# Optimization experiments

Hardware: AMD Instinct MI355X
Metric: run time of the kernel (lower is better)

Reference implementation:

```python
import jax, jax.numpy as jnp
import numpy as np

B, S, D, H = 8, 1024, 1024, 16
DH = D // H
LN_EPS = 1e-5
SLOPE = 0.01  # nn.LeakyReLU default negative_slope


def _ln(x, g, b):
    m = x.mean(-1, keepdims=True)
    v = ((x - m) ** 2).mean(-1, keepdims=True)
    return (x - m) / jnp.sqrt(v + LN_EPS) * g + b


def _leaky(x):
    return jnp.where(x >= 0, x, SLOPE * x)


def setup_inputs() -> dict:
    key = jax.random.key(0)
    ks = jax.random.split(key, 6)
    q = jax.random.normal(ks[0], (B, S, D), dtype=jnp.float32)
    masks = jnp.ones((B, S), dtype=jnp.int32)  # all-valid mask (masked_fill is a no-op)
    w1 = jax.random.normal(ks[1], (D, D), dtype=jnp.float32) * 0.02
    b1 = jnp.zeros((D,), jnp.float32)
    w2 = jax.random.normal(ks[2], (D, D), dtype=jnp.float32) * 0.02
    b2 = jnp.zeros((D,), jnp.float32)
    ones = jnp.ones((D,), jnp.float32)
    zeros = jnp.zeros((D,), jnp.float32)
    return dict(q=q, masks=masks,
                w1=w1, b1=b1, ln1_g=ones, ln1_b=zeros,
                w2=w2, b2=b2, ln2_g=ones, ln2_b=zeros,
                anf_g=ones, anf_b=zeros,
                an1_g=ones, an1_b=zeros,
                an2_g=ones, an2_b=zeros)


def reference(q, masks, w1, b1, ln1_g, ln1_b, w2, b2, ln2_g, ln2_b,
              anf_g, anf_b, an1_g, an1_b, an2_g, an2_b):
    # --- multi-head cosine-similarity attention (k = v = q, no projections) ---
    qh = q.reshape(B, S, H, DH).transpose(0, 2, 1, 3)  # (B,H,S,DH) == separate_heads
    qn = qh / jnp.clip(jnp.linalg.norm(qh, axis=-1, keepdims=True), 1e-8)
    # cosine similarity scores, softmax over keys
    w = jax.nn.softmax(jnp.einsum('bhqd,bhkd->bhqk', qn, qn), axis=-1)
    # masked_fill AFTER softmax (faithful to source: mask per (batch, query))
    w = jnp.where(masks[:, None, :, None] == 0, jnp.float32(-1e9), w)
    heads = jnp.einsum('bhqk,bhkd->bhqd', w, qh)
    attn = heads.transpose(0, 2, 1, 3).reshape(B, S, D)  # concat_heads
    # --- add_norm1 (dropout=0.5 but eval mode => identity) ---
    y1 = _ln(q + attn, an1_g, an1_b)
    # --- PositionWiseFFN: Linear->LN->LeakyReLU x2, then internal AddNorm ---
    h = _leaky(_ln(y1 @ w1 + b1, ln1_g, ln1_b))
    y = _leaky(_ln(h @ w2 + b2, ln2_g, ln2_b))
    y2 = _ln(y1 + y, anf_g, anf_b)
    # --- add_norm2 ---
    return _ln(y1 + y2, an2_g, an2_b)
```

## Files before the change

kernel.cpp:

```cpp
#include <hip/hip_runtime.h>
#include <hip/hip_bf16.h>

#define BB 8
#define SS 1024
#define DD 1024
#define HH 16

typedef __attribute__((ext_vector_type(8))) short short8;
typedef __attribute__((ext_vector_type(8))) __bf16 bf16x8;
typedef __attribute__((ext_vector_type(4))) float f32x4;

__device__ inline float bf2f(unsigned short h){
  unsigned u = ((unsigned)h) << 16;
  return __builtin_bit_cast(float, u);
}
__device__ inline unsigned short f2bf(float f){
  unsigned u = __builtin_bit_cast(unsigned, f);
  u += 0x7fffu + ((u >> 16) & 1u);
  return (unsigned short)(u >> 16);
}
__device__ inline f32x4 mfma16(short8 a, short8 b, f32x4 c){
  return __builtin_amdgcn_mfma_f32_16x16x32_bf16(
      __builtin_bit_cast(bf16x8, a), __builtin_bit_cast(bf16x8, b), c, 0, 0, 0);
}
__device__ inline void gld_lds16(const unsigned short* g, unsigned short* l){
  __builtin_amdgcn_global_load_lds((const __attribute__((address_space(1))) void*)g,
      (__attribute__((address_space(3))) void*)l, 16, 0, 0);
}

__global__ __launch_bounds__(256) void prep_w(const float* __restrict__ w1,
                                              const float* __restrict__ w2,
                                              unsigned short* __restrict__ w1T,
                                              unsigned short* __restrict__ w2T){
  __shared__ float tile[64][65];
  const float* src = blockIdx.z ? w2 : w1;
  unsigned short* dst = blockIdx.z ? w2T : w1T;
  int k0 = blockIdx.x * 64, n0 = blockIdx.y * 64;
  int tx = threadIdx.x & 63, ty = threadIdx.x >> 6;
#pragma unroll
  for (int r = 0; r < 16; ++r)
    tile[ty + 4*r][tx] = src[(k0 + ty + 4*r) * DD + n0 + tx];
  __syncthreads();
#pragma unroll
  for (int r = 0; r < 16; ++r)
    dst[(n0 + ty + 4*r) * DD + k0 + tx] = f2bf(tile[tx][ty + 4*r]);
}

__global__ __launch_bounds__(256) void prep_q(const float* __restrict__ q,
                                              unsigned short* __restrict__ kf,
                                              unsigned short* __restrict__ vf,
                                              unsigned short* __restrict__ qb){
  __shared__ float tile[64][65];
  __shared__ float rinv[64];
  int bh = blockIdx.x >> 4, st = blockIdx.x & 15;
  int b = bh >> 4, h = bh & 15;
  int t = threadIdx.x;
  int tx = t & 63, ty = t >> 6;
  int srow = b * SS + st * 64;
#pragma unroll
  for (int r = 0; r < 16; ++r)
    tile[ty + 4*r][tx] = q[(size_t)(srow + ty + 4*r) * DD + h * 64 + tx];
  __syncthreads();
  {
    int s = t >> 2, p = t & 3;
    float ssum = 0.f;
#pragma unroll
    for (int i = 0; i < 16; ++i){ float v = tile[s][p*16 + i]; ssum += v * v; }
    ssum += __shfl_xor(ssum, 1);
    ssum += __shfl_xor(ssum, 2);
    if (p == 0) rinv[s] = 1.0f / fmaxf(sqrtf(ssum), 1e-8f);
  }
  __syncthreads();
#pragma unroll
  for (int r = 0; r < 16; ++r)
    qb[(size_t)(srow + ty + 4*r) * DD + h * 64 + tx] = f2bf(tile[ty + 4*r][tx]);
#pragma unroll
  for (int v = 0; v < 2; ++v){
    int idx = t * 2 + v;
    int c_l = idx >> 6, lane = idx & 63;
    int g2 = c_l >> 2, c = (c_l >> 1) & 1, hf = c_l & 1;
    int lrq = lane & 15, lgq = lane >> 4;
    int s = g2 * 32 + (lrq >> 2) * 8 + c * 4 + (lrq & 3);
    int d0 = hf * 32 + lgq * 8;
    float rv = rinv[s] * 1.20112240878645f;
    short8 o;
#pragma unroll
    for (int e = 0; e < 8; ++e) o[e] = (short)f2bf(tile[s][d0 + e] * rv);
    *(short8*)(kf + ((size_t)(bh * 128 + st * 8 + c_l) * 64 + lane) * 8) = o;
  }
#pragma unroll
  for (int v = 0; v < 2; ++v){
    int idx = t * 2 + v;
    int kt2 = idx >> 8, db = (idx >> 6) & 3, lane = idx & 63;
    int d = db * 16 + (lane & 15);
    int k0 = kt2 * 32 + (lane >> 4) * 8;
    short8 o;
#pragma unroll
    for (int e = 0; e < 8; ++e) o[e] = (short)f2bf(tile[k0 + e][d]);
    *(short8*)(vf + ((size_t)((bh * 32 + st * 2 + kt2) * 4 + db) * 512 + lane * 8)) = o;
  }
}

#define NPH 16
__global__ __launch_bounds__(512, 4) void attn_kern(const unsigned short* __restrict__ kf,
                                                    const unsigned short* __restrict__ vf,
                                                    const int* __restrict__ masks,
                                                    unsigned short* __restrict__ attnb){
  __shared__ unsigned short Kb[3][8][512];
  __shared__ unsigned short Vb[3][8][512];
  __shared__ int anym;
  const int bh = blockIdx.x, b = bh >> 4, h = bh & 15;
  const int by = blockIdx.y;
  const int t = threadIdx.x, w = t >> 6, l = t & 63;
  const int lr = l & 15, lg = l >> 4;
  if (t == 0) anym = 0;
  __syncthreads();
  if (t < 256 && masks[b * SS + by * 256 + t] == 0) anym = 1;

  short8 aQ[2][2];
#pragma unroll
  for (int c = 0; c < 2; ++c)
#pragma unroll
    for (int hf = 0; hf < 2; ++hf)
      aQ[c][hf] = *(const short8*)(kf +
          ((size_t)(bh * 128 + (by * 8 + w) * 4 + c * 2 + hf) * 64 + l) * 8);

  const short ONEB = (short)0x3F80;
  const short8 ones = {ONEB, ONEB, ONEB, ONEB, ONEB, ONEB, ONEB, ONEB};

#define STAGE(ph, bf) do {                                                            \
    if (w < 4){                                                                       \
      gld_lds16(kf + ((size_t)(bh * 128 + (2*(ph)) * 4 + w) * 64 + l) * 8,            \
                &Kb[bf][w][0]);                                                       \
      gld_lds16(kf + ((size_t)(bh * 128 + (2*(ph)+1) * 4 + w) * 64 + l) * 8,          \
                &Kb[bf][4 + w][0]);                                                   \
    } else {                                                                          \
      gld_lds16(vf + ((size_t)((bh * 32 + 2*(ph)) * 4 + (w - 4)) * 512 + l * 8),      \
                &Vb[bf][w - 4][0]);                                                   \
      gld_lds16(vf + ((size_t)((bh * 32 + 2*(ph)+1) * 4 + (w - 4)) * 512 + l * 8),    \
                &Vb[bf][4 + (w - 4)][0]);                                             \
    }                                                                                 \
  } while (0)

  STAGE(0, 0);
  STAGE(1, 1);
  asm volatile("s_waitcnt vmcnt(2) lgkmcnt(0)" ::: "memory");
  __builtin_amdgcn_s_barrier();

  f32x4 o[2][4] = {};
  f32x4 rsacc[2] = {};

  for (int ph = 0; ph < NPH; ++ph){
    const int cur = ph % 3;
    if (ph + 2 < NPH) STAGE(ph + 2, (ph + 2) % 3);
#pragma unroll
    for (int gi = 0; gi < 2; ++gi){
      short8 bK[2][2];
#pragma unroll
      for (int c = 0; c < 2; ++c)
#pragma unroll
        for (int hf = 0; hf < 2; ++hf)
          bK[c][hf] = *(const short8*)&Kb[cur][gi * 4 + c * 2 + hf][l * 8];
      f32x4 sc[2][2];
#pragma unroll
      for (int qc = 0; qc < 2; ++qc)
#pragma unroll
        for (int c = 0; c < 2; ++c){
          f32x4 z = {0.f, 0.f, 0.f, 0.f};
          z = mfma16(bK[c][0], aQ[qc][0], z);
          z = mfma16(bK[c][1], aQ[qc][1], z);
          sc[qc][c] = z;
        }
      bf16x8 pav[2];
#pragma unroll
      for (int qc = 0; qc < 2; ++qc)
#pragma unroll
        for (int c = 0; c < 2; ++c)
#pragma unroll
          for (int j = 0; j < 4; ++j){
            float x = sc[qc][c][j], pv;
            asm("v_exp_f32 %0, %1" : "=v"(pv) : "v"(x));
            pav[qc][c * 4 + j] = (__bf16)pv;
          }
      short8 pa0 = __builtin_bit_cast(short8, pav[0]);
      short8 pa1 = __builtin_bit_cast(short8, pav[1]);
      rsacc[0] = mfma16(pa0, ones, rsacc[0]);
      rsacc[1] = mfma16(pa1, ones, rsacc[1]);
#pragma unroll
      for (int db = 0; db < 4; ++db){
        short8 bV = *(const short8*)&Vb[cur][gi * 4 + db][l * 8];
        o[0][db] = mfma16(pa0, bV, o[0][db]);
        o[1][db] = mfma16(pa1, bV, o[1][db]);
      }
    }
    if (ph + 1 < NPH){
      asm volatile("s_waitcnt lgkmcnt(0)" ::: "memory");
      if (ph + 2 < NPH) asm volatile("s_waitcnt vmcnt(2)" ::: "memory");
      else              asm volatile("s_waitcnt vmcnt(0)" ::: "memory");
      __builtin_amdgcn_s_barrier();
    }
  }

#pragma unroll
  for (int qc = 0; qc < 2; ++qc){
    float invj[4];
#pragma unroll
    for (int j = 0; j < 4; ++j) invj[j] = 1.0f / rsacc[qc][j];
#pragma unroll
    for (int db = 0; db < 4; ++db)
#pragma unroll
      for (int j = 0; j < 4; ++j){
        int qrow = by * 256 + w * 32 + lg * 8 + qc * 4 + j;
        float val = o[qc][db][j] * invj[j];
        if (anym && masks[b * SS + qrow] == 0){
          float vs = 0.f;
          for (int kt = 0; kt < 32; ++kt)
            for (int lgp = 0; lgp < 4; ++lgp){
              const unsigned short* vp = vf +
                  ((size_t)((bh * 32 + kt) * 4 + db) * 512 + (lgp * 16 + lr) * 8);
              for (int e = 0; e < 8; ++e) vs += bf2f(vp[e]);
            }
          val = -1e9f * vs;
        }
        attnb[(size_t)(b * SS + qrow) * DD + h * 64 + db * 16 + lr] = f2bf(val);
      }
  }
#undef STAGE
}

__device__ inline float2 block_reduce2(float a, float bq){
  __shared__ float sm[8];
#pragma unroll
  for (int off = 1; off < 64; off <<= 1){
    a += __shfl_xor(a, off);
    bq += __shfl_xor(bq, off);
  }
  int w = threadIdx.x >> 6;
  if ((threadIdx.x & 63) == 0){ sm[2*w] = a; sm[2*w + 1] = bq; }
  __syncthreads();
  float2 r;
  r.x = sm[0] + sm[2] + sm[4] + sm[6];
  r.y = sm[1] + sm[3] + sm[5] + sm[7];
  __syncthreads();
  return r;
}

__global__ __launch_bounds__(256) void addnorm1(const unsigned short* __restrict__ qb,
                                                const unsigned short* __restrict__ attnb,
                                                const float* __restrict__ g,
                                                const float* __restrict__ bt,
                                                unsigned short* __restrict__ y1b){
  int row = blockIdx.x, t = threadIdx.x;
  ushort4 qv = *(const ushort4*)(qb + (size_t)row * DD + t * 4);
  ushort4 av = *(const ushort4*)(attnb + (size_t)row * DD + t * 4);
  float x[4] = { bf2f(qv.x) + bf2f(av.x), bf2f(qv.y) + bf2f(av.y),
                 bf2f(qv.z) + bf2f(av.z), bf2f(qv.w) + bf2f(av.w) };
  float s = 0.f, ssq = 0.f;
#pragma unroll
  for (int i = 0; i < 4; ++i){ s += x[i]; ssq += x[i] * x[i]; }
  float2 r = block_reduce2(s, ssq);
  float m = r.x * (1.0f / DD);
  float rs = rsqrtf(r.y * (1.0f / DD) - m * m + 1e-5f);
  float4 gv = *(const float4*)(g + t * 4);
  float4 bv = *(const float4*)(bt + t * 4);
  float y[4] = { (x[0]-m)*rs*gv.x + bv.x, (x[1]-m)*rs*gv.y + bv.y,
                 (x[2]-m)*rs*gv.z + bv.z, (x[3]-m)*rs*gv.w + bv.w };
  ushort4 ob = { f2bf(y[0]), f2bf(y[1]), f2bf(y[2]), f2bf(y[3]) };
  *(ushort4*)(y1b + (size_t)row * DD + t * 4) = ob;
}

__global__ __launch_bounds__(256, 2) void gemm_bias(const unsigned short* __restrict__ X,
                                                    const unsigned short* __restrict__ WT,
                                                    const float* __restrict__ bias,
                                                    unsigned short* __restrict__ out){
  __shared__ unsigned short As[3][128 * 32];
  __shared__ unsigned short Bs[3][128 * 32];
  int t = threadIdx.x, l = t & 63, w = t >> 6;
  int wm = w >> 1, wn = w & 1;
  int lr = l & 15, lg = l >> 4;
  int bm = blockIdx.x * 128, bn = blockIdx.y * 128;
  f32x4 acc[4][4] = {};
  int r = t >> 2, cb = (t & 3) * 8;

#define GSTAGE(kt, bf) do {                                                        \
    gld_lds16(X  + (size_t)(bm +      r) * 1024 + (kt) * 32 + cb,                  \
              &As[bf][w * 512]);                                                   \
    gld_lds16(X  + (size_t)(bm + 64 + r) * 1024 + (kt) * 32 + cb,                  \
              &As[bf][2048 + w * 512]);                                            \
    gld_lds16(WT + (size_t)(bn +      r) * 1024 + (kt) * 32 + cb,                  \
              &Bs[bf][w * 512]);                                                   \
    gld_lds16(WT + (size_t)(bn + 64 + r) * 1024 + (kt) * 32 + cb,                  \
              &Bs[bf][2048 + w * 512]);                                            \
  } while (0)

  GSTAGE(0, 0);
  GSTAGE(1, 1);
  asm volatile("s_waitcnt vmcnt(4)" ::: "memory");
  __builtin_amdgcn_s_barrier();

  for (int kt = 0; kt < 32; ++kt){
    const int cur = kt % 3;
    if (kt + 2 < 32) GSTAGE(kt + 2, (kt + 2) % 3);
    short8 aA[4], bB[4];
#pragma unroll
    for (int i = 0; i < 4; ++i)
      aA[i] = *(const short8*)&As[cur][(wm * 64 + i * 16 + lr) * 32 + lg * 8];
#pragma unroll
    for (int i = 0; i < 4; ++i)
      bB[i] = *(const short8*)&Bs[cur][(wn * 64 + i * 16 + lr) * 32 + lg * 8];
#pragma unroll
    for (int mi = 0; mi < 4; ++mi)
#pragma unroll
      for (int ni = 0; ni < 4; ++ni)
        acc[mi][ni] = mfma16(aA[mi], bB[ni], acc[mi][ni]);
    if (kt + 1 < 32){
      asm volatile("s_waitcnt lgkmcnt(0)" ::: "memory");
      if (kt + 2 < 32) asm volatile("s_waitcnt vmcnt(4)" ::: "memory");
      else             asm volatile("s_waitcnt vmcnt(0)" ::: "memory");
      __builtin_amdgcn_s_barrier();
    }
  }
#undef GSTAGE
#pragma unroll
  for (int ni = 0; ni < 4; ++ni){
    int col = bn + wn * 64 + ni * 16 + lr;
    float bv = bias[col];
#pragma unroll
    for (int mi = 0; mi < 4; ++mi){
      int row0 = bm + wm * 64 + mi * 16 + lg * 4;
#pragma unroll
      for (int j = 0; j < 4; ++j)
        out[(size_t)(row0 + j) * 1024 + col] = f2bf(acc[mi][ni][j] + bv);
    }
  }
}

__global__ __launch_bounds__(256) void ln_leaky(const unsigned short* __restrict__ in,
                                                const float* __restrict__ g,
                                                const float* __restrict__ bt,
                                                unsigned short* __restrict__ out){
  int row = blockIdx.x, t = threadIdx.x;
  ushort4 iv = *(const ushort4*)(in + (size_t)row * DD + t * 4);
  float x[4] = { bf2f(iv.x), bf2f(iv.y), bf2f(iv.z), bf2f(iv.w) };
  float s = 0.f, ssq = 0.f;
#pragma unroll
  for (int i = 0; i < 4; ++i){ s += x[i]; ssq += x[i] * x[i]; }
  float2 r = block_reduce2(s, ssq);
  float m = r.x * (1.0f / DD);
  float rs = rsqrtf(r.y * (1.0f / DD) - m * m + 1e-5f);
  float4 gv = *(const float4*)(g + t * 4);
  float4 bv = *(const float4*)(bt + t * 4);
  ushort4 ov;
  {
    float v0 = (x[0]-m)*rs*gv.x + bv.x; v0 = v0 >= 0.f ? v0 : 0.01f*v0; ov.x = f2bf(v0);
    float v1 = (x[1]-m)*rs*gv.y + bv.y; v1 = v1 >= 0.f ? v1 : 0.01f*v1; ov.y = f2bf(v1);
    float v2 = (x[2]-m)*rs*gv.z + bv.z; v2 = v2 >= 0.f ? v2 : 0.01f*v2; ov.z = f2bf(v2);
    float v3 = (x[3]-m)*rs*gv.w + bv.w; v3 = v3 >= 0.f ? v3 : 0.01f*v3; ov.w = f2bf(v3);
  }
  *(ushort4*)(out + (size_t)row * DD + t * 4) = ov;
}

__global__ __launch_bounds__(256) void final_kern(const unsigned short* __restrict__ g2,
                                                  const unsigned short* __restrict__ y1,
                                                  const float* __restrict__ ln2g, const float* __restrict__ ln2b,
                                                  const float* __restrict__ anfg, const float* __restrict__ anfb,
                                                  const float* __restrict__ an2g, const float* __restrict__ an2b,
                                                  float* __restrict__ out){
  int row = blockIdx.x, t = threadIdx.x;
  ushort4 iv = *(const ushort4*)(g2 + (size_t)row * DD + t * 4);
  ushort4 y1v = *(const ushort4*)(y1 + (size_t)row * DD + t * 4);
  float x[4] = { bf2f(iv.x), bf2f(iv.y), bf2f(iv.z), bf2f(iv.w) };
  float yy1[4] = { bf2f(y1v.x), bf2f(y1v.y), bf2f(y1v.z), bf2f(y1v.w) };
  float s = 0.f, ssq = 0.f;
#pragma unroll
  for (int i = 0; i < 4; ++i){ s += x[i]; ssq += x[i]*x[i]; }
  float2 r = block_reduce2(s, ssq);
  float m = r.x * (1.0f / DD);
  float rs = rsqrtf(r.y * (1.0f / DD) - m*m + 1e-5f);
  float4 gv = *(const float4*)(ln2g + t * 4);
  float4 bv = *(const float4*)(ln2b + t * 4);
  float y[4] = { (x[0]-m)*rs*gv.x + bv.x, (x[1]-m)*rs*gv.y + bv.y,
                 (x[2]-m)*rs*gv.z + bv.z, (x[3]-m)*rs*gv.w + bv.w };
#pragma unroll
  for (int i = 0; i < 4; ++i) y[i] = y[i] >= 0.f ? y[i] : 0.01f*y[i];

  float tv[4]; s = 0.f; ssq = 0.f;
#pragma unroll
  for (int i = 0; i < 4; ++i){ tv[i] = yy1[i] + y[i]; s += tv[i]; ssq += tv[i]*tv[i]; }
  r = block_reduce2(s, ssq);
  m = r.x * (1.0f / DD);
  rs = rsqrtf(r.y * (1.0f / DD) - m*m + 1e-5f);
  gv = *(const float4*)(anfg + t * 4);
  bv = *(const float4*)(anfb + t * 4);
  float y2[4] = { (tv[0]-m)*rs*gv.x + bv.x, (tv[1]-m)*rs*gv.y + bv.y,
                  (tv[2]-m)*rs*gv.z + bv.z, (tv[3]-m)*rs*gv.w + bv.w };

  float u[4]; s = 0.f; ssq = 0.f;
#pragma unroll
  for (int i = 0; i < 4; ++i){ u[i] = yy1[i] + y2[i]; s += u[i]; ssq += u[i]*u[i]; }
  r = block_reduce2(s, ssq);
  m = r.x * (1.0f / DD);
  rs = rsqrtf(r.y * (1.0f / DD) - m*m + 1e-5f);
  gv = *(const float4*)(an2g + t * 4);
  bv = *(const float4*)(an2b + t * 4);
  float4 ov = { (u[0]-m)*rs*gv.x + bv.x, (u[1]-m)*rs*gv.y + bv.y,
                (u[2]-m)*rs*gv.z + bv.z, (u[3]-m)*rs*gv.w + bv.w };
  *(float4*)(out + (size_t)row * DD + t * 4) = ov;
}

extern "C" void kernel_launch(void* const* d_in, const int* in_sizes, int n_in,
                              void* d_out, int out_size, void* d_ws, size_t ws_size,
                              hipStream_t stream){
  const float* q    = (const float*)d_in[0];
  const int* masks  = (const int*)d_in[1];
  const float* w1   = (const float*)d_in[2];
  const float* b1   = (const float*)d_in[3];
  const float* ln1g = (const float*)d_in[4];
  const float* ln1b = (const float*)d_in[5];
  const float* w2   = (const float*)d_in[6];
  const float* b2   = (const float*)d_in[7];
  const float* ln2g = (const float*)d_in[8];
  const float* ln2b = (const float*)d_in[9];
  const float* anfg = (const float*)d_in[10];
  const float* anfb = (const float*)d_in[11];
  const float* an1g = (const float*)d_in[12];
  const float* an1b = (const float*)d_in[13];
  const float* an2g = (const float*)d_in[14];
  const float* an2b = (const float*)d_in[15];

  char* ws = (char*)d_ws;
  unsigned short* w1T  = (unsigned short*)(ws + 0);
  unsigned short* w2T  = (unsigned short*)(ws + 2097152);
  unsigned short* kf   = (unsigned short*)(ws + 4194304);
  unsigned short* vf   = (unsigned short*)(ws + 20971520);
  unsigned short* attn = (unsigned short*)(ws + 37748736);
  unsigned short* y1b  = (unsigned short*)(ws + 54525952);
  unsigned short* qb   = (unsigned short*)(ws + 71303168);
  unsigned short* g1   = kf;
  unsigned short* hbuf = vf;
  unsigned short* g2   = attn;
  float* outp = (float*)d_out;

  prep_w<<<dim3(16, 16, 2), 256, 0, stream>>>(w1, w2, w1T, w2T);
  prep_q<<<dim3(2048), 256, 0, stream>>>(q, kf, vf, qb);
  attn_kern<<<dim3(128, 4), 512, 0, stream>>>(kf, vf, masks, attn);
  addnorm1<<<dim3(8192), 256, 0, stream>>>(qb, attn, an1g, an1b, y1b);
  gemm_bias<<<dim3(64, 8), 256, 0, stream>>>(y1b, w1T, b1, g1);
  ln_leaky<<<dim3(8192), 256, 0, stream>>>(g1, ln1g, ln1b, hbuf);
  gemm_bias<<<dim3(64, 8), 256, 0, stream>>>(hbuf, w2T, b2, g2);
  final_kern<<<dim3(8192), 256, 0, stream>>>(g2, y1b, ln2g, ln2b, anfg, anfb, an2g, an2b, outp);
}
```

Before: 155.1 us.

## Stage GEMM output through LDS, vectorize row-norm kernels to two rows per block

The GEMM epilogue now writes bias-added bf16 results into the shared-memory buffer, then copies them out as coalesced 16-byte row stores instead of scattered 2-byte stores. The MFMA loop is wrapped in s_setprio to favour the math waves. The three layer-norm kernels now process two rows per 256-thread block with 8-element vector loads and a half-block reduction, halving their grid size. The added barriers and LDS round trip cost a little time in the GEMM epilogue.

```diff
diff --git a/kernel.cpp b/kernel.cpp
--- a/kernel.cpp
+++ b/kernel.cpp
@@ -228,7 +228,7 @@
 #undef STAGE
 }
 
-__device__ inline float2 block_reduce2(float a, float bq){
+__device__ inline float2 br2(float a, float bq){
   __shared__ float sm[8];
 #pragma unroll
   for (int off = 1; off < 64; off <<= 1){
@@ -236,11 +236,12 @@
     bq += __shfl_xor(bq, off);
   }
   int w = threadIdx.x >> 6;
-  if ((threadIdx.x & 63) == 0){ sm[2*w] = a; sm[2*w + 1] = bq; }
-  __syncthreads();
+  if ((threadIdx.x & 63) == 0){ sm[w * 2] = a; sm[w * 2 + 1] = bq; }
+  __syncthreads();
+  int base = (threadIdx.x >> 7) * 4;
   float2 r;
-  r.x = sm[0] + sm[2] + sm[4] + sm[6];
-  r.y = sm[1] + sm[3] + sm[5] + sm[7];
+  r.x = sm[base] + sm[base + 2];
+  r.y = sm[base + 1] + sm[base + 3];
   __syncthreads();
   return r;
 }
@@ -250,31 +251,34 @@
                                                 const float* __restrict__ g,
                                                 const float* __restrict__ bt,
                                                 unsigned short* __restrict__ y1b){
-  int row = blockIdx.x, t = threadIdx.x;
-  ushort4 qv = *(const ushort4*)(qb + (size_t)row * DD + t * 4);
-  ushort4 av = *(const ushort4*)(attnb + (size_t)row * DD + t * 4);
-  float x[4] = { bf2f(qv.x) + bf2f(av.x), bf2f(qv.y) + bf2f(av.y),
-                 bf2f(qv.z) + bf2f(av.z), bf2f(qv.w) + bf2f(av.w) };
-  float s = 0.f, ssq = 0.f;
-#pragma unroll
-  for (int i = 0; i < 4; ++i){ s += x[i]; ssq += x[i] * x[i]; }
-  float2 r = block_reduce2(s, ssq);
+  int rg = threadIdx.x >> 7, tt = threadIdx.x & 127;
+  int row = blockIdx.x * 2 + rg;
+  short8 qv = *(const short8*)(qb + (size_t)row * DD + tt * 8);
+  short8 av = *(const short8*)(attnb + (size_t)row * DD + tt * 8);
+  float x[8]; float s = 0.f, ssq = 0.f;
+#pragma unroll
+  for (int i = 0; i < 8; ++i){
+    x[i] = bf2f((unsigned short)qv[i]) + bf2f((unsigned short)av[i]);
+    s += x[i]; ssq += x[i] * x[i];
+  }
+  float2 r = br2(s, ssq);
   float m = r.x * (1.0f / DD);
   float rs = rsqrtf(r.y * (1.0f / DD) - m * m + 1e-5f);
-  float4 gv = *(const float4*)(g + t * 4);
-  float4 bv = *(const float4*)(bt + t * 4);
-  float y[4] = { (x[0]-m)*rs*gv.x + bv.x, (x[1]-m)*rs*gv.y + bv.y,
-                 (x[2]-m)*rs*gv.z + bv.z, (x[3]-m)*rs*gv.w + bv.w };
-  ushort4 ob = { f2bf(y[0]), f2bf(y[1]), f2bf(y[2]), f2bf(y[3]) };
-  *(ushort4*)(y1b + (size_t)row * DD + t * 4) = ob;
+  float4 g0 = *(const float4*)(g + tt * 8), g1 = *(const float4*)(g + tt * 8 + 4);
+  float4 b0 = *(const float4*)(bt + tt * 8), b1 = *(const float4*)(bt + tt * 8 + 4);
+  float gg[8] = {g0.x,g0.y,g0.z,g0.w,g1.x,g1.y,g1.z,g1.w};
+  float bb[8] = {b0.x,b0.y,b0.z,b0.w,b1.x,b1.y,b1.z,b1.w};
+  short8 ob;
+#pragma unroll
+  for (int i = 0; i < 8; ++i) ob[i] = (short)f2bf((x[i]-m)*rs*gg[i] + bb[i]);
+  *(short8*)(y1b + (size_t)row * DD + tt * 8) = ob;
 }
 
 __global__ __launch_bounds__(256, 2) void gemm_bias(const unsigned short* __restrict__ X,
                                                     const unsigned short* __restrict__ WT,
                                                     const float* __restrict__ bias,
                                                     unsigned short* __restrict__ out){
-  __shared__ unsigned short As[3][128 * 32];
-  __shared__ unsigned short Bs[3][128 * 32];
+  __shared__ unsigned short LDSB[24576];
   int t = threadIdx.x, l = t & 63, w = t >> 6;
   int wm = w >> 1, wn = w & 1;
   int lr = l & 15, lg = l >> 4;
@@ -282,15 +286,17 @@
   f32x4 acc[4][4] = {};
   int r = t >> 2, cb = (t & 3) * 8;
 
+#define ASP(bf) (LDSB + (bf) * 4096)
+#define BSP(bf) (LDSB + 12288 + (bf) * 4096)
 #define GSTAGE(kt, bf) do {                                                        \
     gld_lds16(X  + (size_t)(bm +      r) * 1024 + (kt) * 32 + cb,                  \
-              &As[bf][w * 512]);                                                   \
+              ASP(bf) + w * 512);                                                  \
     gld_lds16(X  + (size_t)(bm + 64 + r) * 1024 + (kt) * 32 + cb,                  \
-              &As[bf][2048 + w * 512]);                                            \
+              ASP(bf) + 2048 + w * 512);                                           \
     gld_lds16(WT + (size_t)(bn +      r) * 1024 + (kt) * 32 + cb,                  \
-              &Bs[bf][w * 512]);                                                   \
+              BSP(bf) + w * 512);                                                  \
     gld_lds16(WT + (size_t)(bn + 64 + r) * 1024 + (kt) * 32 + cb,                  \
-              &Bs[bf][2048 + w * 512]);                                            \
+              BSP(bf) + 2048 + w * 512);                                           \
   } while (0)
 
   GSTAGE(0, 0);
@@ -304,15 +310,17 @@
     short8 aA[4], bB[4];
 #pragma unroll
     for (int i = 0; i < 4; ++i)
-      aA[i] = *(const short8*)&As[cur][(wm * 64 + i * 16 + lr) * 32 + lg * 8];
+      aA[i] = *(const short8*)(ASP(cur) + (wm * 64 + i * 16 + lr) * 32 + lg * 8);
 #pragma unroll
     for (int i = 0; i < 4; ++i)
-      bB[i] = *(const short8*)&Bs[cur][(wn * 64 + i * 16 + lr) * 32 + lg * 8];
+      bB[i] = *(const short8*)(BSP(cur) + (wn * 64 + i * 16 + lr) * 32 + lg * 8);
+    __builtin_amdgcn_s_setprio(1);
 #pragma unroll
     for (int mi = 0; mi < 4; ++mi)
 #pragma unroll
       for (int ni = 0; ni < 4; ++ni)
         acc[mi][ni] = mfma16(aA[mi], bB[ni], acc[mi][ni]);
+    __builtin_amdgcn_s_setprio(0);
     if (kt + 1 < 32){
       asm volatile("s_waitcnt lgkmcnt(0)" ::: "memory");
       if (kt + 2 < 32) asm volatile("s_waitcnt vmcnt(4)" ::: "memory");
@@ -321,43 +329,63 @@
     }
   }
 #undef GSTAGE
+
+  asm volatile("s_waitcnt lgkmcnt(0)" ::: "memory");
+  __builtin_amdgcn_s_barrier();
 #pragma unroll
   for (int ni = 0; ni < 4; ++ni){
-    int col = bn + wn * 64 + ni * 16 + lr;
-    float bv = bias[col];
+    int col = wn * 64 + ni * 16 + lr;
+    float bv = bias[bn + col];
 #pragma unroll
     for (int mi = 0; mi < 4; ++mi){
-      int row0 = bm + wm * 64 + mi * 16 + lg * 4;
+      int row0 = wm * 64 + mi * 16 + lg * 4;
 #pragma unroll
       for (int j = 0; j < 4; ++j)
-        out[(size_t)(row0 + j) * 1024 + col] = f2bf(acc[mi][ni][j] + bv);
+        LDSB[(row0 + j) * 128 + col] = f2bf(acc[mi][ni][j] + bv);
     }
   }
+  asm volatile("s_waitcnt lgkmcnt(0)" ::: "memory");
+  __builtin_amdgcn_s_barrier();
+#pragma unroll
+  for (int i = 0; i < 8; ++i){
+    int idx = t + i * 256;
+    int row = idx >> 4;
+    int c8  = idx & 15;
+    short8 v = *(const short8*)&LDSB[row * 128 + c8 * 8];
+    *(short8*)(out + (size_t)(bm + row) * 1024 + bn + c8 * 8) = v;
+  }
+#undef ASP
+#undef BSP
 }
 
 __global__ __launch_bounds__(256) void ln_leaky(const unsigned short* __restrict__ in,
                                                 const float* __restrict__ g,
                                                 const float* __restrict__ bt,
                                                 unsigned short* __restrict__ out){
-  int row = blockIdx.x, t = threadIdx.x;
-  ushort4 iv = *(const ushort4*)(in + (size_t)row * DD + t * 4);
-  float x[4] = { bf2f(iv.x), bf2f(iv.y), bf2f(iv.z), bf2f(iv.w) };
-  float s = 0.f, ssq = 0.f;
-#pragma unroll
-  for (int i = 0; i < 4; ++i){ s += x[i]; ssq += x[i] * x[i]; }
-  float2 r = block_reduce2(s, ssq);
+  int rg = threadIdx.x >> 7, tt = threadIdx.x & 127;
+  int row = blockIdx.x * 2 + rg;
+  short8 iv = *(const short8*)(in + (size_t)row * DD + tt * 8);
+  float x[8]; float s = 0.f, ssq = 0.f;
+#pragma unroll
+  for (int i = 0; i < 8; ++i){
+    x[i] = bf2f((unsigned short)iv[i]);
+    s += x[i]; ssq += x[i] * x[i];
+  }
+  float2 r = br2(s, ssq);
   float m = r.x * (1.0f / DD);
   float rs = rsqrtf(r.y * (1.0f / DD) - m * m + 1e-5f);
-  float4 gv = *(const float4*)(g + t * 4);
-  float4 bv = *(const float4*)(bt + t * 4);
-  ushort4 ov;
-  {
-    float v0 = (x[0]-m)*rs*gv.x + bv.x; v0 = v0 >= 0.f ? v0 : 0.01f*v0; ov.x = f2bf(v0);
-    float v1 = (x[1]-m)*rs*gv.y + bv.y; v1 = v1 >= 0.f ? v1 : 0.01f*v1; ov.y = f2bf(v1);
-    float v2 = (x[2]-m)*rs*gv.z + bv.z; v2 = v2 >= 0.f ? v2 : 0.01f*v2; ov.z = f2bf(v2);
-    float v3 = (x[3]-m)*rs*gv.w + bv.w; v3 = v3 >= 0.f ? v3 : 0.01f*v3; ov.w = f2bf(v3);
-  }
-  *(ushort4*)(out + (size_t)row * DD + t * 4) = ov;
+  float4 g0 = *(const float4*)(g + tt * 8), g1 = *(const float4*)(g + tt * 8 + 4);
+  float4 b0 = *(const float4*)(bt + tt * 8), b1 = *(const float4*)(bt + tt * 8 + 4);
+  float gg[8] = {g0.x,g0.y,g0.z,g0.w,g1.x,g1.y,g1.z,g1.w};
+  float bb[8] = {b0.x,b0.y,b0.z,b0.w,b1.x,b1.y,b1.z,b1.w};
+  short8 ov;
+#pragma unroll
+  for (int i = 0; i < 8; ++i){
+    float v = (x[i]-m)*rs*gg[i] + bb[i];
+    v = v >= 0.f ? v : 0.01f * v;
+    ov[i] = (short)f2bf(v);
+  }
+  *(short8*)(out + (size_t)row * DD + tt * 8) = ov;
 }
 
 __global__ __launch_bounds__(256) void final_kern(const unsigned short* __restrict__ g2,
@@ -366,46 +394,62 @@
                                                   const float* __restrict__ anfg, const float* __restrict__ anfb,
                                                   const float* __restrict__ an2g, const float* __restrict__ an2b,
                                                   float* __restrict__ out){
-  int row = blockIdx.x, t = threadIdx.x;
-  ushort4 iv = *(const ushort4*)(g2 + (size_t)row * DD + t * 4);
-  ushort4 y1v = *(const ushort4*)(y1 + (size_t)row * DD + t * 4);
-  float x[4] = { bf2f(iv.x), bf2f(iv.y), bf2f(iv.z), bf2f(iv.w) };
-  float yy1[4] = { bf2f(y1v.x), bf2f(y1v.y), bf2f(y1v.z), bf2f(y1v.w) };
-  float s = 0.f, ssq = 0.f;
-#pragma unroll
-  for (int i = 0; i < 4; ++i){ s += x[i]; ssq += x[i]*x[i]; }
-  float2 r = block_reduce2(s, ssq);
+  int rg = threadIdx.x >> 7, tt = threadIdx.x & 127;
+  int row = blockIdx.x * 2 + rg;
+  short8 iv = *(const short8*)(g2 + (size_t)row * DD + tt * 8);
+  short8 yv = *(const short8*)(y1 + (size_t)row * DD + tt * 8);
+  float x[8], yy1[8]; float s = 0.f, ssq = 0.f;
+#pragma unroll
+  for (int i = 0; i < 8; ++i){
+    x[i] = bf2f((unsigned short)iv[i]);
+    yy1[i] = bf2f((unsigned short)yv[i]);
+    s += x[i]; ssq += x[i] * x[i];
+  }
+  float2 r = br2(s, ssq);
   float m = r.x * (1.0f / DD);
-  float rs = rsqrtf(r.y * (1.0f / DD) - m*m + 1e-5f);
-  float4 gv = *(const float4*)(ln2g + t * 4);
-  float4 bv = *(const float4*)(ln2b + t * 4);
-  float y[4] = { (x[0]-m)*rs*gv.x + bv.x, (x[1]-m)*rs*gv.y + bv.y,
-                 (x[2]-m)*rs*gv.z + bv.z, (x[3]-m)*rs*gv.w + bv.w };
-#pragma unroll
-  for (int i = 0; i < 4; ++i) y[i] = y[i] >= 0.f ? y[i] : 0.01f*y[i];
-
-  float tv[4]; s = 0.f; ssq = 0.f;
-#pragma unroll
-  for (int i = 0; i < 4; ++i){ tv[i] = yy1[i] + y[i]; s += tv[i]; ssq += tv[i]*tv[i]; }
-  r = block_reduce2(s, ssq);
+  float rs = rsqrtf(r.y * (1.0f / DD) - m * m + 1e-5f);
+  float4 p0, p1;
+  p0 = *(const float4*)(ln2g + tt * 8); p1 = *(const float4*)(ln2g + tt * 8 + 4);
+  float gg[8] = {p0.x,p0.y,p0.z,p0.w,p1.x,p1.y,p1.z,p1.w};
+  p0 = *(const float4*)(ln2b + tt * 8); p1 = *(const float4*)(ln2b + tt * 8 + 4);
+  float bb[8] = {p0.x,p0.y,p0.z,p0.w,p1.x,p1.y,p1.z,p1.w};
+  float y[8];
+#pragma unroll
+  for (int i = 0; i < 8; ++i){
+    float v = (x[i]-m)*rs*gg[i] + bb[i];
+    y[i] = v >= 0.f ? v : 0.01f * v;
+  }
+
+  float tv[8]; s = 0.f; ssq = 0.f;
+#pragma unroll
+  for (int i = 0; i < 8; ++i){ tv[i] = yy1[i] + y[i]; s += tv[i]; ssq += tv[i]*tv[i]; }
+  r = br2(s, ssq);
   m = r.x * (1.0f / DD);
   rs = rsqrtf(r.y * (1.0f / DD) - m*m + 1e-5f);
-  gv = *(const float4*)(anfg + t * 4);
-  bv = *(const float4*)(anfb + t * 4);
-  float y2[4] = { (tv[0]-m)*rs*gv.x + bv.x, (tv[1]-m)*rs*gv.y + bv.y,
-                  (tv[2]-m)*rs*gv.z + bv.z, (tv[3]-m)*rs*gv.w + bv.w };
-
-  float u[4]; s = 0.f; ssq = 0.f;
-#pragma unroll
-  for (int i = 0; i < 4; ++i){ u[i] = yy1[i] + y2[i]; s += u[i]; ssq += u[i]*u[i]; }
-  r = block_reduce2(s, ssq);
+  p0 = *(const float4*)(anfg + tt * 8); p1 = *(const float4*)(anfg + tt * 8 + 4);
+  float gg2[8] = {p0.x,p0.y,p0.z,p0.w,p1.x,p1.y,p1.z,p1.w};
+  p0 = *(const float4*)(anfb + tt * 8); p1 = *(const float4*)(anfb + tt * 8 + 4);
+  float bb2[8] = {p0.x,p0.y,p0.z,p0.w,p1.x,p1.y,p1.z,p1.w};
+  float y2[8];
+#pragma unroll
+  for (int i = 0; i < 8; ++i) y2[i] = (tv[i]-m)*rs*gg2[i] + bb2[i];
+
+  float u[8]; s = 0.f; ssq = 0.f;
+#pragma unroll
+  for (int i = 0; i < 8; ++i){ u[i] = yy1[i] + y2[i]; s += u[i]; ssq += u[i]*u[i]; }
+  r = br2(s, ssq);
   m = r.x * (1.0f / DD);
   rs = rsqrtf(r.y * (1.0f / DD) - m*m + 1e-5f);
-  gv = *(const float4*)(an2g + t * 4);
-  bv = *(const float4*)(an2b + t * 4);
-  float4 ov = { (u[0]-m)*rs*gv.x + bv.x, (u[1]-m)*rs*gv.y + bv.y,
-                (u[2]-m)*rs*gv.z + bv.z, (u[3]-m)*rs*gv.w + bv.w };
-  *(float4*)(out + (size_t)row * DD + t * 4) = ov;
+  p0 = *(const float4*)(an2g + tt * 8); p1 = *(const float4*)(an2g + tt * 8 + 4);
+  float gg3[8] = {p0.x,p0.y,p0.z,p0.w,p1.x,p1.y,p1.z,p1.w};
+  p0 = *(const float4*)(an2b + tt * 8); p1 = *(const float4*)(an2b + tt * 8 + 4);
+  float bb3[8] = {p0.x,p0.y,p0.z,p0.w,p1.x,p1.y,p1.z,p1.w};
+  float4 o0 = { (u[0]-m)*rs*gg3[0] + bb3[0], (u[1]-m)*rs*gg3[1] + bb3[1],
+                (u[2]-m)*rs*gg3[2] + bb3[2], (u[3]-m)*rs*gg3[3] + bb3[3] };
+  float4 o1 = { (u[4]-m)*rs*gg3[4] + bb3[4], (u[5]-m)*rs*gg3[5] + bb3[5],
+                (u[6]-m)*rs*gg3[6] + bb3[6], (u[7]-m)*rs*gg3[7] + bb3[7] };
+  *(float4*)(out + (size_t)row * DD + tt * 8) = o0;
+  *(float4*)(out + (size_t)row * DD + tt * 8 + 4) = o1;
 }
 
 extern "C" void kernel_launch(void* const* d_in, const int* in_sizes, int n_in,
@@ -444,9 +488,9 @@
   prep_w<<<dim3(16, 16, 2), 256, 0, stream>>>(w1, w2, w1T, w2T);
   prep_q<<<dim3(2048), 256, 0, stream>>>(q, kf, vf, qb);
   attn_kern<<<dim3(128, 4), 512, 0, stream>>>(kf, vf, masks, attn);
-  addnorm1<<<dim3(8192), 256, 0, stream>>>(qb, attn, an1g, an1b, y1b);
+  addnorm1<<<dim3(4096), 256, 0, stream>>>(qb, attn, an1g, an1b, y1b);
   gemm_bias<<<dim3(64, 8), 256, 0, stream>>>(y1b, w1T, b1, g1);
-  ln_leaky<<<dim3(8192), 256, 0, stream>>>(g1, ln1g, ln1b, hbuf);
+  ln_leaky<<<dim3(4096), 256, 0, stream>>>(g1, ln1g, ln1b, hbuf);
   gemm_bias<<<dim3(64, 8), 256, 0, stream>>>(hbuf, w2T, b2, g2);
-  final_kern<<<dim3(8192), 256, 0, stream>>>(g2, y1b, ln2g, ln2b, anfg, anfb, an2g, an2b, outp);
-}
+  final_kern<<<dim3(4096), 256, 0, stream>>>(g2, y1b, ln2g, ln2b, anfg, anfb, an2g, an2b, outp);
+}
```

Measured after the change: 144.1 us. 7.0% less time.
